# Kernel optimization log

Measured on AMD Instinct MI355X. Metric: run time of the kernel, lower is better.

The kernel has to match this reference:

```python
import jax, jax.numpy as jnp
import numpy as np


def _lstm(x, h0, c0, Wx, Wh, b):
    """Keras-order LSTM (gates i,f,c,o). x: [B,T,E] -> hidden seq [B,T,H]."""
    xw = jnp.einsum('bte,eg->btg', x, Wx) + b  # precompute input projections

    def step(carry, xw_t):
        h, c = carry
        z = xw_t + h @ Wh
        i, f, g, o = jnp.split(z, 4, axis=-1)
        c = jax.nn.sigmoid(f) * c + jax.nn.sigmoid(i) * jnp.tanh(g)
        h = jax.nn.sigmoid(o) * jnp.tanh(c)
        return (h, c), h

    _, hs = jax.lax.scan(step, (h0, c0), jnp.swapaxes(xw, 0, 1))
    return jnp.swapaxes(hs, 0, 1)


def setup_inputs() -> dict:
    key = jax.random.key(0)
    ks = jax.random.split(key, 16)
    V_IN = V_OUT = 32000
    E = 512      # embedding_dim
    H = 512      # encoder hidden_units per direction
    D = 2 * H    # decoder state width (matches BiLSTM output / attention dims)
    B, T_IN, T_OUT = 4, 128, 128
    s = 0.02

    def w(k, shape):
        return jax.random.normal(k, shape, jnp.float32) * s

    return {
        'input_seq': jax.random.randint(ks[0], (B, T_IN), 0, V_IN, jnp.int32),
        'output_seq': jax.random.randint(ks[1], (B, T_OUT), 0, V_OUT, jnp.int32),
        'enc_emb': w(ks[2], (V_IN, E)),
        'dec_emb': w(ks[3], (V_OUT, E)),
        'Wx_f': w(ks[4], (E, 4 * H)), 'Wh_f': w(ks[5], (H, 4 * H)), 'b_f': jnp.zeros((4 * H,), jnp.float32),
        'Wx_b': w(ks[6], (E, 4 * H)), 'Wh_b': w(ks[7], (H, 4 * H)), 'b_b': jnp.zeros((4 * H,), jnp.float32),
        'Wx_d': w(ks[8], (E, 4 * D)), 'Wh_d': w(ks[9], (D, 4 * D)), 'b_d': jnp.zeros((4 * D,), jnp.float32),
        'attn_scale': w(ks[10], (D,)),
        'Wo': w(ks[11], (D, V_OUT)), 'bo': jnp.zeros((V_OUT,), jnp.float32),
    }


def reference(input_seq, output_seq, enc_emb, dec_emb,
              Wx_f, Wh_f, b_f, Wx_b, Wh_b, b_b,
              Wx_d, Wh_d, b_d, attn_scale, Wo, bo):
    B = input_seq.shape[0]
    H = Wh_f.shape[0]
    D = 2 * H

    # --- encoder: BiLSTM, return_sequences=True ---
    enc_x = enc_emb[input_seq]                       # [B,Tin,E]
    z = jnp.zeros((B, H), jnp.float32)
    fwd = _lstm(enc_x, z, z, Wx_f, Wh_f, b_f)        # [B,Tin,H]
    bwd = _lstm(enc_x[:, ::-1], z, z, Wx_b, Wh_b, b_b)[:, ::-1]
    enc_out = jnp.concatenate([fwd, bwd], axis=-1)   # [B,Tin,2H]

    # --- decoder: LSTMCell-driven RNN, init state = last encoder output ---
    dec_x = dec_emb[output_seq]                      # [B,Tout,E]
    h0 = enc_out[:, -1, :]                           # [B,D]
    c0 = jnp.zeros((B, D), jnp.float32)
    dec_out = _lstm(dec_x, h0, c0, Wx_d, Wh_d, b_d)  # [B,Tout,D]

    # --- additive (Bahdanau) attention: query=dec_out, key=value=enc_out ---
    scores = jnp.einsum(
        'btsd,d->bts',
        jnp.tanh(dec_out[:, :, None, :] + enc_out[:, None, :, :]),
        attn_scale)                                  # [B,Tout,Tin]
    wts = jax.nn.softmax(scores, axis=-1)
    attn = jnp.einsum('bts,bsd->btd', wts, enc_out)  # [B,Tout,D]

    # --- output dense + softmax over vocab ---
    return jax.nn.softmax(attn @ Wo + bo, axis=-1)   # [B,Tout,V_out]
```

## Files before the change

kernel.cpp:

```cpp
#include <hip/hip_runtime.h>


typedef __attribute__((ext_vector_type(8))) short bf16x8;
typedef __attribute__((ext_vector_type(4))) float f32x4;

__device__ __forceinline__ short f2bf(float f) {
  unsigned u = __builtin_bit_cast(unsigned, f);
  u += 0x7fffu + ((u >> 16) & 1u);
  return (short)(u >> 16);
}
__device__ __forceinline__ float b2f(short s) {
  unsigned u = ((unsigned)(unsigned short)s) << 16;
  return __builtin_bit_cast(float, u);
}
__device__ __forceinline__ float sigf(float x) { return 1.f / (1.f + __expf(-x)); }
__device__ __forceinline__ float tanhf_fast(float x) {
  x = fminf(fmaxf(x, -15.f), 15.f);
  float e = __expf(2.f * x);
  return (e - 1.f) / (e + 1.f);
}

__device__ __forceinline__ unsigned ld_coh(const unsigned* p) {
  return __hip_atomic_load(p, __ATOMIC_RELAXED, __HIP_MEMORY_SCOPE_AGENT);
}
__device__ __forceinline__ void st_coh(unsigned* p, unsigned v) {
  __hip_atomic_store(p, v, __ATOMIC_RELAXED, __HIP_MEMORY_SCOPE_AGENT);
}

#define OFF_HBF   ((size_t)0)
#define OFF_HBB   (OFF_HBF + 2*2048*4)
#define OFF_HBD   (OFF_HBB + 2*2048*4)
#define OFF_ENCX  (OFF_HBD + 2*4096*4)
#define OFF_DECX  (OFF_ENCX + (size_t)64*512*8*2)
#define OFF_WXF   (OFF_DECX + (size_t)64*512*8*2)
#define OFF_WXB   (OFF_WXF + (size_t)512*2048*2)
#define OFF_WXD   (OFF_WXB + (size_t)512*2048*2)
#define OFF_WOS   (OFF_WXD + (size_t)512*4096*2)
#define OFF_XWF   (OFF_WOS + (size_t)1024*32000*2)
#define OFF_XWB   (OFF_XWF + (size_t)512*2048*4)
#define OFF_XWD   (OFF_XWB + (size_t)512*2048*4)
#define OFF_ENCO  (OFF_XWD + (size_t)512*4096*4)
#define OFF_ENCT  (OFF_ENCO + (size_t)4*128*1024*4)
#define OFF_DECO  (OFF_ENCT + (size_t)4*128*1024*4)
#define OFF_ATTN  (OFF_DECO + (size_t)4*128*1024*4)
#define OFF_LOG   (OFF_ATTN + (size_t)128*512*8*2)
#define WS_NEED   (OFF_LOG + (size_t)512*32000*2)

__device__ __forceinline__ void gather_body(const int* seq, const float* emb,
                                            short* dst, int bx, int by) {
  int m  = by * 64 + (threadIdx.x & 63);
  int e8 = bx * 4 + (threadIdx.x >> 6);
  int id = seq[m];
  const float* src = emb + (size_t)id * 512 + e8 * 8;
  bf16x8 v;
#pragma unroll
  for (int j = 0; j < 8; ++j) v[j] = f2bf(src[j]);
  *(bf16x8*)(dst + ((size_t)e8 * 512 + m) * 8) = v;
}

__device__ __forceinline__ void swz_body(const float* W, short* dst, int N,
                                         int k8, int n) {
  const float* src = W + (size_t)k8 * 8 * N + n;
  bf16x8 v;
#pragma unroll
  for (int j = 0; j < 8; ++j) v[j] = f2bf(src[(size_t)j * N]);
  *(bf16x8*)(dst + ((size_t)k8 * N + n) * 8) = v;
}

__device__ __forceinline__ void gemm_body(const short* __restrict__ A,
                                          const short* __restrict__ B,
                                          float* Cf, short* Cb,
                                          int M, int N, int K,
                                          int bx, int by, bool bf16out) {
  const int wv = threadIdx.x >> 6, lane = threadIdx.x & 63;
  const int q = lane >> 4, l15 = lane & 15;
  const int m0 = by * 128 + (wv >> 1) * 64;
  const int n0 = bx * 128 + (wv & 1) * 64;
  f32x4 acc[4][4];
#pragma unroll
  for (int i = 0; i < 4; ++i)
#pragma unroll
    for (int j = 0; j < 4; ++j) acc[i][j] = (f32x4){0.f, 0.f, 0.f, 0.f};
  const int KS = K >> 5;
  for (int ks = 0; ks < KS; ++ks) {
    const size_t k8 = (size_t)(ks * 4 + q);
    const short* Ap = A + (k8 * M + m0 + l15) * 8;
    const short* Bp = B + (k8 * N + n0 + l15) * 8;
    bf16x8 av[4], bv[4];
#pragma unroll
    for (int i = 0; i < 4; ++i) av[i] = *(const bf16x8*)(Ap + i * 128);
#pragma unroll
    for (int j = 0; j < 4; ++j) bv[j] = *(const bf16x8*)(Bp + j * 128);
#pragma unroll
    for (int i = 0; i < 4; ++i)
#pragma unroll
      for (int j = 0; j < 4; ++j)
        acc[i][j] = __builtin_amdgcn_mfma_f32_16x16x32_bf16(av[i], bv[j], acc[i][j], 0, 0, 0);
  }
#pragma unroll
  for (int i = 0; i < 4; ++i)
#pragma unroll
    for (int j = 0; j < 4; ++j)
#pragma unroll
      for (int r = 0; r < 4; ++r) {
        size_t idx = (size_t)(m0 + i * 16 + q * 4 + r) * N + (n0 + j * 16 + l15);
        if (bf16out) Cb[idx] = f2bf(acc[i][j][r]);
        else         Cf[idx] = acc[i][j][r];
      }
}

__global__ __launch_bounds__(256) void prep(
    const int* __restrict__ iseq, const int* __restrict__ oseq,
    const float* __restrict__ enc_emb, const float* __restrict__ dec_emb,
    const float* __restrict__ Wx_f, const float* __restrict__ Wx_b,
    const float* __restrict__ Wx_d,
    short* encx, short* decx, short* wxf_s, short* wxb_s, short* wxd_s) {
  int bid = blockIdx.x;
  if (bid < 128)        { gather_body(iseq, enc_emb, encx, bid & 15, bid >> 4); return; }
  if (bid < 256)        { int s = bid - 128;  gather_body(oseq, dec_emb, decx, s & 15, s >> 4); return; }
  if (bid < 768)        { int s = bid - 256;  swz_body(Wx_f, wxf_s, 2048, s >> 3, (s & 7) * 256 + threadIdx.x); return; }
  if (bid < 1280)       { int s = bid - 768;  swz_body(Wx_b, wxb_s, 2048, s >> 3, (s & 7) * 256 + threadIdx.x); return; }
  { int s = bid - 1280; swz_body(Wx_d, wxd_s, 4096, s >> 4, (s & 15) * 256 + threadIdx.x); }
}

__global__ __launch_bounds__(256) void xw_enc_gemm(
    const short* __restrict__ encx, const short* __restrict__ wxf_s,
    const short* __restrict__ wxb_s, float* xw_f, float* xw_b) {
  gemm_body(encx, blockIdx.z ? wxb_s : wxf_s, blockIdx.z ? xw_b : xw_f,
            nullptr, 512, 2048, 512, blockIdx.x, blockIdx.y, false);
}

__global__ __launch_bounds__(256, 1) void lstm_enc_fused(
    const float* __restrict__ Wh_f, const float* __restrict__ Wh_b,
    const float* __restrict__ xw_f, const float* __restrict__ xw_b,
    const float* __restrict__ b_f, const float* __restrict__ b_b,
    unsigned* hb_f, unsigned* hb_b, float* enc_out, float* encT,
    const short* __restrict__ decx, const short* __restrict__ wxd_s,
    float* xw_d, const float* __restrict__ Wo, short* wo_s) {
  const int bid = blockIdx.x;
  const int tid = threadIdx.x;
  if (bid >= 192) {
    int sb = bid - 192;
    int k8 = sb / 125, nb = sb - k8 * 125;
    swz_body(Wo, wo_s, 32000, k8, nb * 256 + tid);
    return;
  }
  if (bid >= 64) {
    int gb = bid - 64;
    gemm_body(decx, wxd_s, xw_d, nullptr, 512, 4096, 512, gb & 31, gb >> 5, false);
    return;
  }
  const int dir = bid >> 5;
  const int u0  = (bid & 31) * 16;
  const int w = tid >> 6, lane = tid & 63;
  const int q = lane >> 4, l15 = lane & 15;
  const float* Wh   = dir ? Wh_b : Wh_f;
  const float* xw   = dir ? xw_b : xw_f;
  const float* bias = dir ? b_b : b_f;
  unsigned* hb = dir ? hb_b : hb_f;

  __shared__ short hs[5][520];
  __shared__ float zb[4][4][16];
  __shared__ float cb[4][16];
  if (tid < 64) {
    cb[tid >> 4][tid & 15] = 0.f;
    st_coh(hb + (tid >> 4) * 512 + u0 + (tid & 15), 1u << 16);
  }
  for (int k = tid; k < 520; k += 256) hs[4][k] = 0;

  const int col = w * 512 + u0 + l15;
  const float bcol = bias[col];
  bf16x8 wfrag[16];
#pragma unroll
  for (int ks = 0; ks < 16; ++ks) {
    bf16x8 v;
#pragma unroll
    for (int jj = 0; jj < 8; ++jj) {
      int k = ks * 32 + q * 8 + jj;
      v[jj] = f2bf(Wh[(size_t)k * 2048 + col]);
    }
    wfrag[ks] = v;
  }
  const short* hp = hs[(l15 < 4) ? l15 : 4];
  float xwv[4];
  if (q == 0) {
    int tx0 = dir ? 127 : 0;
#pragma unroll
    for (int r = 0; r < 4; ++r) xwv[r] = xw[((size_t)(r * 128 + tx0)) * 2048 + col];
  }
  __syncthreads();

#pragma unroll 1
  for (int t = 0; t < 128; ++t) {
    const unsigned exp_ = (unsigned)(t + 1);
    const unsigned* src = hb + (t & 1) * 2048;
    unsigned v[8];
    bool ok;
    int guard = 0;
    do {
#pragma unroll
      for (int j = 0; j < 8; ++j) v[j] = ld_coh(src + j * 256 + tid);
      ok = true;
#pragma unroll
      for (int j = 0; j < 8; ++j) ok &= ((v[j] >> 16) == exp_);
      if (!ok) __builtin_amdgcn_s_sleep(1);
    } while (!ok && ++guard < (1 << 14));
#pragma unroll
    for (int j = 0; j < 8; ++j) {
      unsigned idx = j * 256 + tid;
      hs[idx >> 9][idx & 511] = (short)(v[j] & 0xffffu);
    }
    __syncthreads();

    f32x4 a0 = (f32x4){0.f, 0.f, 0.f, 0.f}, a1 = a0;
#pragma unroll
    for (int ks = 0; ks < 16; ks += 2) {
      bf16x8 f0 = *(const bf16x8*)(hp + ks * 32 + q * 8);
      bf16x8 f1 = *(const bf16x8*)(hp + (ks + 1) * 32 + q * 8);
      a0 = __builtin_amdgcn_mfma_f32_16x16x32_bf16(f0, wfrag[ks], a0, 0, 0, 0);
      a1 = __builtin_amdgcn_mfma_f32_16x16x32_bf16(f1, wfrag[ks + 1], a1, 0, 0, 0);
    }
    const int tx = dir ? (127 - t) : t;
    if (q == 0) {
#pragma unroll
      for (int r = 0; r < 4; ++r) zb[w][r][l15] = a0[r] + a1[r] + xwv[r] + bcol;
      if (t < 127) {
        int txn = dir ? (126 - t) : (t + 1);
#pragma unroll
        for (int r = 0; r < 4; ++r) xwv[r] = xw[((size_t)(r * 128 + txn)) * 2048 + col];
      }
    }
    __syncthreads();
    if (tid < 64) {
      int b = tid >> 4, u = tid & 15;
      float zi = zb[0][b][u], zf = zb[1][b][u], zg = zb[2][b][u], zo = zb[3][b][u];
      float c = sigf(zf) * cb[b][u] + sigf(zi) * tanhf_fast(zg);
      cb[b][u] = c;
      float h = sigf(zo) * tanhf_fast(c);
      if (t < 127)
        st_coh(hb + ((t + 1) & 1) * 2048 + b * 512 + u0 + u,
               ((unsigned)(t + 2) << 16) | (unsigned short)f2bf(h));
      int d = dir * 512 + u0 + u;
      enc_out[((size_t)(b * 128 + tx)) * 1024 + d] = h;
      encT[((size_t)(b * 1024 + d)) * 128 + tx] = h;
    }
  }
}

__global__ __launch_bounds__(256, 1) void lstm_dec(
    const float* __restrict__ Wh_d, const float* __restrict__ xw_d,
    const float* __restrict__ b_d, const float* __restrict__ enc_out,
    unsigned* hb, float* dec_out) {
  const int u0  = blockIdx.x * 16;
  const int tid = threadIdx.x;
  const int w = tid >> 6, lane = tid & 63;
  const int q = lane >> 4, l15 = lane & 15;

  __shared__ short hs[5][1032];
  __shared__ float zb[4][4][16];
  __shared__ float cb[4][16];
  if (tid < 64) {
    int b = tid >> 4, u = tid & 15;
    cb[b][u] = 0.f;
    float h0 = enc_out[((size_t)(b * 128 + 127)) * 1024 + u0 + u];
    st_coh(hb + b * 1024 + u0 + u, (1u << 16) | (unsigned short)f2bf(h0));
  }
  for (int k = tid; k < 1032; k += 256) hs[4][k] = 0;

  const int col = w * 1024 + u0 + l15;
  const float bcol = b_d[col];
  bf16x8 wfrag[32];
#pragma unroll
  for (int ks = 0; ks < 32; ++ks) {
    bf16x8 v;
#pragma unroll
    for (int jj = 0; jj < 8; ++jj) {
      int k = ks * 32 + q * 8 + jj;
      v[jj] = f2bf(Wh_d[(size_t)k * 4096 + col]);
    }
    wfrag[ks] = v;
  }
  const short* hp = hs[(l15 < 4) ? l15 : 4];
  float xwv[4];
  if (q == 0) {
#pragma unroll
    for (int r = 0; r < 4; ++r) xwv[r] = xw_d[((size_t)(r * 128)) * 4096 + col];
  }
  __syncthreads();

#pragma unroll 1
  for (int t = 0; t < 128; ++t) {
    const unsigned exp_ = (unsigned)(t + 1);
    const unsigned* src = hb + (t & 1) * 4096;
    unsigned v[16];
    bool ok;
    int guard = 0;
    do {
#pragma unroll
      for (int j = 0; j < 16; ++j) v[j] = ld_coh(src + j * 256 + tid);
      ok = true;
#pragma unroll
      for (int j = 0; j < 16; ++j) ok &= ((v[j] >> 16) == exp_);
      if (!ok) __builtin_amdgcn_s_sleep(1);
    } while (!ok && ++guard < (1 << 14));
#pragma unroll
    for (int j = 0; j < 16; ++j) {
      unsigned idx = j * 256 + tid;
      hs[idx >> 10][idx & 1023] = (short)(v[j] & 0xffffu);
    }
    __syncthreads();

    f32x4 a0 = (f32x4){0.f, 0.f, 0.f, 0.f}, a1 = a0;
#pragma unroll
    for (int ks = 0; ks < 32; ks += 2) {
      bf16x8 f0 = *(const bf16x8*)(hp + ks * 32 + q * 8);
      bf16x8 f1 = *(const bf16x8*)(hp + (ks + 1) * 32 + q * 8);
      a0 = __builtin_amdgcn_mfma_f32_16x16x32_bf16(f0, wfrag[ks], a0, 0, 0, 0);
      a1 = __builtin_amdgcn_mfma_f32_16x16x32_bf16(f1, wfrag[ks + 1], a1, 0, 0, 0);
    }
    if (q == 0) {
#pragma unroll
      for (int r = 0; r < 4; ++r) zb[w][r][l15] = a0[r] + a1[r] + xwv[r] + bcol;
      if (t < 127) {
#pragma unroll
        for (int r = 0; r < 4; ++r) xwv[r] = xw_d[((size_t)(r * 128 + t + 1)) * 4096 + col];
      }
    }
    __syncthreads();
    if (tid < 64) {
      int b = tid >> 4, u = tid & 15;
      float zi = zb[0][b][u], zf = zb[1][b][u], zg = zb[2][b][u], zo = zb[3][b][u];
      float c = sigf(zf) * cb[b][u] + sigf(zi) * tanhf_fast(zg);
      cb[b][u] = c;
      float h = sigf(zo) * tanhf_fast(c);
      if (t < 127)
        st_coh(hb + ((t + 1) & 1) * 4096 + b * 1024 + u0 + u,
               ((unsigned)(t + 2) << 16) | (unsigned short)f2bf(h));
      dec_out[((size_t)(b * 128 + t)) * 1024 + u0 + u] = h;
    }
  }
}

__global__ __launch_bounds__(256) void attention(
    const float* __restrict__ dec_out, const float* __restrict__ enc_out,
    const float* __restrict__ encT, const float* __restrict__ scale,
    short* __restrict__ attn_swz) {
  const int m = blockIdx.x, b = m >> 7, tid = threadIdx.x;
  __shared__ float dec_s[1024], scl_s[1024];
  __shared__ float red[256], wts[128], sred[2];
  for (int d = tid; d < 1024; d += 256) {
    dec_s[d] = dec_out[(size_t)m * 1024 + d];
    scl_s[d] = scale[d];
  }
  __syncthreads();
  const int s = tid & 127, half = tid >> 7;
  float sc = 0.f;
  const float* ep = encT + (size_t)b * 1024 * 128 + s;
  for (int d = half * 512; d < half * 512 + 512; ++d)
    sc += tanhf_fast(dec_s[d] + ep[(size_t)d * 128]) * scl_s[d];
  red[tid] = sc;
  __syncthreads();
  float v = 0.f;
  if (tid < 128) { v = red[tid] + red[tid + 128]; wts[tid] = v; }
  __syncthreads();
  if (tid < 64) {
    float mx = fmaxf(wts[tid], wts[tid + 64]);
    for (int off = 32; off; off >>= 1) mx = fmaxf(mx, __shfl_down(mx, off));
    if (tid == 0) sred[0] = mx;
  }
  __syncthreads();
  const float MX = sred[0];
  if (tid < 128) { v = __expf(v - MX); wts[tid] = v; }
  __syncthreads();
  if (tid < 64) {
    float sm = wts[tid] + wts[tid + 64];
    for (int off = 32; off; off >>= 1) sm += __shfl_down(sm, off);
    if (tid == 0) sred[1] = sm;
  }
  __syncthreads();
  const float inv = 1.f / sred[1];
  if (tid < 128) wts[tid] = v * inv;
  __syncthreads();
#pragma unroll
  for (int kk = 0; kk < 4; ++kk) {
    int d = tid + kk * 256;
    float a = 0.f;
    for (int ss = 0; ss < 128; ++ss)
      a += wts[ss] * enc_out[((size_t)(b * 128 + ss)) * 1024 + d];
    attn_swz[((size_t)(d >> 3) * 512 + m) * 8 + (d & 7)] = f2bf(a);
  }
}

__global__ __launch_bounds__(256) void gemm_wo(const short* __restrict__ attn_s,
                                               const short* __restrict__ wo_s,
                                               short* logits) {
  gemm_body(attn_s, wo_s, nullptr, logits, 512, 32000, 1024,
            blockIdx.x, blockIdx.y, true);
}

__global__ __launch_bounds__(256) void softmax_out(const short* __restrict__ logits,
                                                   const float* __restrict__ bo,
                                                   float* __restrict__ out) {
  const int m = blockIdx.x, tid = threadIdx.x;
  __shared__ float red[256];
  const short* lp = logits + (size_t)m * 32000;
  float mx = -1e30f;
  for (int n = tid; n < 32000; n += 256) mx = fmaxf(mx, b2f(lp[n]) + bo[n]);
  red[tid] = mx;
  __syncthreads();
  for (int s2 = 128; s2 > 0; s2 >>= 1) {
    if (tid < s2) red[tid] = fmaxf(red[tid], red[tid + s2]);
    __syncthreads();
  }
  const float M = red[0];
  __syncthreads();
  float sm = 0.f;
  for (int n = tid; n < 32000; n += 256) sm += __expf(b2f(lp[n]) + bo[n] - M);
  red[tid] = sm;
  __syncthreads();
  for (int s2 = 128; s2 > 0; s2 >>= 1) {
    if (tid < s2) red[tid] += red[tid + s2];
    __syncthreads();
  }
  const float inv = 1.f / red[0];
  for (int n = tid; n < 32000; n += 256)
    out[(size_t)m * 32000 + n] = __expf(b2f(lp[n]) + bo[n] - M) * inv;
}

extern "C" void kernel_launch(void* const* d_in, const int* in_sizes, int n_in,
                              void* d_out, int out_size, void* d_ws, size_t ws_size,
                              hipStream_t stream) {
  (void)in_sizes; (void)n_in; (void)out_size;
  if (ws_size < WS_NEED) return;

  const int*   input_seq  = (const int*)d_in[0];
  const int*   output_seq = (const int*)d_in[1];
  const float* enc_emb    = (const float*)d_in[2];
  const float* dec_emb    = (const float*)d_in[3];
  const float* Wx_f = (const float*)d_in[4];
  const float* Wh_f = (const float*)d_in[5];
  const float* b_f  = (const float*)d_in[6];
  const float* Wx_b = (const float*)d_in[7];
  const float* Wh_b = (const float*)d_in[8];
  const float* b_b  = (const float*)d_in[9];
  const float* Wx_d = (const float*)d_in[10];
  const float* Wh_d = (const float*)d_in[11];
  const float* b_d  = (const float*)d_in[12];
  const float* attn_scale = (const float*)d_in[13];
  const float* Wo   = (const float*)d_in[14];
  const float* bo   = (const float*)d_in[15];
  float* out = (float*)d_out;

  char* ws = (char*)d_ws;
  unsigned* hbf   = (unsigned*)(ws + OFF_HBF);
  unsigned* hbb   = (unsigned*)(ws + OFF_HBB);
  unsigned* hbd   = (unsigned*)(ws + OFF_HBD);
  short* encx     = (short*)(ws + OFF_ENCX);
  short* decx     = (short*)(ws + OFF_DECX);
  short* wxf_s    = (short*)(ws + OFF_WXF);
  short* wxb_s    = (short*)(ws + OFF_WXB);
  short* wxd_s    = (short*)(ws + OFF_WXD);
  short* wo_s     = (short*)(ws + OFF_WOS);
  float* xw_f     = (float*)(ws + OFF_XWF);
  float* xw_b     = (float*)(ws + OFF_XWB);
  float* xw_d     = (float*)(ws + OFF_XWD);
  float* enc_out  = (float*)(ws + OFF_ENCO);
  float* encT     = (float*)(ws + OFF_ENCT);
  float* dec_out  = (float*)(ws + OFF_DECO);
  short* attn_s   = (short*)(ws + OFF_ATTN);
  short* logits   = (short*)(ws + OFF_LOG);


  prep<<<2304, 256, 0, stream>>>(input_seq, output_seq, enc_emb, dec_emb,
                                 Wx_f, Wx_b, Wx_d, encx, decx, wxf_s, wxb_s, wxd_s);
  xw_enc_gemm<<<dim3(16, 4, 2), 256, 0, stream>>>(encx, wxf_s, wxb_s, xw_f, xw_b);
  lstm_enc_fused<<<64 + 128 + 16000, 256, 0, stream>>>(
      Wh_f, Wh_b, xw_f, xw_b, b_f, b_b, hbf, hbb, enc_out, encT,
      decx, wxd_s, xw_d, Wo, wo_s);
  lstm_dec<<<64, 256, 0, stream>>>(Wh_d, xw_d, b_d, enc_out, hbd, dec_out);
  attention<<<512, 256, 0, stream>>>(dec_out, enc_out, encT, attn_scale, attn_s);
  gemm_wo<<<dim3(250, 4), 256, 0, stream>>>(attn_s, wo_s, logits);
  softmax_out<<<512, 256, 0, stream>>>(logits, bo, out);
}
```

Measured before the change: 1.175 ms.

## Fuse input projections into LSTM kernels and overlap attention with decoder

Removes the separate input-projection GEMMs and weight swizzles. Each LSTM block now computes its own slice of x·Wx into shared memory before the recurrence. The gate column layout is remapped so each lane holds all four gates (i,f,g,o) for one unit and batch, which removes the zb shared-memory exchange and one __syncthreads per step. The poll loop is double-buffered, and the attention blocks run inside the decoder kernel, spinning on per-timestep published hidden states so attention overlaps the recurrence. The tradeoffs are a longer serial prologue per recurrent block, attention blocks spinning while they occupy CUs, and the risk of deadlock if they cannot all be co-resident with the 64 LSTM blocks.

```diff
diff --git a/kernel.cpp b/kernel.cpp
--- a/kernel.cpp
+++ b/kernel.cpp
@@ -19,7 +19,6 @@
   float e = __expf(2.f * x);
   return (e - 1.f) / (e + 1.f);
 }
-
 __device__ __forceinline__ unsigned ld_coh(const unsigned* p) {
   return __hip_atomic_load(p, __ATOMIC_RELAXED, __HIP_MEMORY_SCOPE_AGENT);
 }
@@ -28,21 +27,15 @@
 }
 
 #define OFF_HBF   ((size_t)0)
-#define OFF_HBB   (OFF_HBF + 2*2048*4)
-#define OFF_HBD   (OFF_HBB + 2*2048*4)
-#define OFF_ENCX  (OFF_HBD + 2*4096*4)
+#define OFF_HBB   (OFF_HBF + (size_t)2*2048*4)
+#define OFF_HBD   (OFF_HBB + (size_t)2*2048*4)
+#define OFF_HBH   (OFF_HBD + (size_t)2*4096*4)
+#define OFF_ENCX  (OFF_HBH + (size_t)128*4*1024*4)
 #define OFF_DECX  (OFF_ENCX + (size_t)64*512*8*2)
-#define OFF_WXF   (OFF_DECX + (size_t)64*512*8*2)
-#define OFF_WXB   (OFF_WXF + (size_t)512*2048*2)
-#define OFF_WXD   (OFF_WXB + (size_t)512*2048*2)
-#define OFF_WOS   (OFF_WXD + (size_t)512*4096*2)
-#define OFF_XWF   (OFF_WOS + (size_t)1024*32000*2)
-#define OFF_XWB   (OFF_XWF + (size_t)512*2048*4)
-#define OFF_XWD   (OFF_XWB + (size_t)512*2048*4)
-#define OFF_ENCO  (OFF_XWD + (size_t)512*4096*4)
+#define OFF_WOS   (OFF_DECX + (size_t)64*512*8*2)
+#define OFF_ENCO  (OFF_WOS + (size_t)1024*32000*2)
 #define OFF_ENCT  (OFF_ENCO + (size_t)4*128*1024*4)
-#define OFF_DECO  (OFF_ENCT + (size_t)4*128*1024*4)
-#define OFF_ATTN  (OFF_DECO + (size_t)4*128*1024*4)
+#define OFF_ATTN  (OFF_ENCT + (size_t)4*128*1024*4)
 #define OFF_LOG   (OFF_ATTN + (size_t)128*512*8*2)
 #define WS_NEED   (OFF_LOG + (size_t)512*32000*2)
 
@@ -67,22 +60,333 @@
   *(bf16x8*)(dst + ((size_t)k8 * N + n) * 8) = v;
 }
 
-__device__ __forceinline__ void gemm_body(const short* __restrict__ A,
-                                          const short* __restrict__ B,
-                                          float* Cf, short* Cb,
-                                          int M, int N, int K,
-                                          int bx, int by, bool bf16out) {
+__global__ __launch_bounds__(256) void prep(const int* __restrict__ iseq,
+                                            const int* __restrict__ oseq,
+                                            const float* __restrict__ enc_emb,
+                                            const float* __restrict__ dec_emb,
+                                            short* encx, short* decx) {
+  int bid = blockIdx.x;
+  if (bid < 128) gather_body(iseq, enc_emb, encx, bid & 15, bid >> 4);
+  else { int s = bid - 128; gather_body(oseq, dec_emb, decx, s & 15, s >> 4); }
+}
+
+__global__ __launch_bounds__(256, 1) void lstm_enc_fused(
+    const float* __restrict__ Wh_f, const float* __restrict__ Wh_b,
+    const float* __restrict__ Wx_f, const float* __restrict__ Wx_b,
+    const float* __restrict__ b_f, const float* __restrict__ b_b,
+    const short* __restrict__ encx,
+    unsigned* hb_f, unsigned* hb_b, float* enc_out, float* encT,
+    const float* __restrict__ Wo, short* wo_s) {
+  const int bid = blockIdx.x, tid = threadIdx.x;
+  if (bid >= 64) {
+    int sb = bid - 64;
+    int k8 = sb / 125, nb = sb - k8 * 125;
+    swz_body(Wo, wo_s, 32000, k8, nb * 256 + tid);
+    return;
+  }
+  __shared__ float xws[512][16];
+  __shared__ short hs[4][528];
+  const int dir = bid >> 5, u0 = (bid & 31) * 16;
+  const int w = tid >> 6, lane = tid & 63, q = lane >> 4, l15 = lane & 15;
+  const int bq = l15 & 3;
+  const int unit = u0 + w * 4 + q;
+  unsigned* hb = dir ? hb_b : hb_f;
+
+  if (l15 < 4) st_coh(hb + l15 * 512 + unit, 1u << 16);
+
+  const int colA = (l15 & 3) * 512 + u0 + w * 4 + (l15 >> 2);
+  const float* Wx   = dir ? Wx_b : Wx_f;
+  const float* bias = dir ? b_b : b_f;
+  const float bcol = bias[colA];
+
+  {
+    bf16x8 bfr[16];
+#pragma unroll
+    for (int ks = 0; ks < 16; ++ks) {
+      bf16x8 v;
+#pragma unroll
+      for (int jj = 0; jj < 8; ++jj)
+        v[jj] = f2bf(Wx[(size_t)(ks * 32 + q * 8 + jj) * 2048 + colA]);
+      bfr[ks] = v;
+    }
+    for (int mt = 0; mt < 32; ++mt) {
+      f32x4 a0 = {0.f,0.f,0.f,0.f}, a1 = a0;
+#pragma unroll
+      for (int ks = 0; ks < 16; ks += 2) {
+        bf16x8 f0 = *(const bf16x8*)(encx + ((size_t)(ks*4 + q) * 512 + mt*16 + l15) * 8);
+        bf16x8 f1 = *(const bf16x8*)(encx + ((size_t)((ks+1)*4 + q) * 512 + mt*16 + l15) * 8);
+        a0 = __builtin_amdgcn_mfma_f32_16x16x32_bf16(f0, bfr[ks], a0, 0, 0, 0);
+        a1 = __builtin_amdgcn_mfma_f32_16x16x32_bf16(f1, bfr[ks+1], a1, 0, 0, 0);
+      }
+#pragma unroll
+      for (int r = 0; r < 4; ++r) xws[mt*16 + q*4 + r][l15] = a0[r] + a1[r] + bcol;
+    }
+  }
+  const float* Wh = dir ? Wh_b : Wh_f;
+  bf16x8 wfrag[16];
+#pragma unroll
+  for (int ks = 0; ks < 16; ++ks) {
+    bf16x8 v;
+#pragma unroll
+    for (int jj = 0; jj < 8; ++jj)
+      v[jj] = f2bf(Wh[(size_t)(ks * 32 + q * 8 + jj) * 2048 + colA]);
+    wfrag[ks] = v;
+  }
+  __syncthreads();
+  float creg = 0.f;
+  f32x4 xwv = *(const f32x4*)&xws[bq * 128 + (dir ? 127 : 0)][q * 4];
+
+#pragma unroll 1
+  for (int t = 0; t < 128; ++t) {
+    const unsigned exp_ = (unsigned)(t + 1);
+    const unsigned* src = hb + (t & 1) * 2048;
+    unsigned pa[8], pb[8];
+#pragma unroll
+    for (int j = 0; j < 8; ++j) pa[j] = ld_coh(src + j * 256 + tid);
+#pragma unroll
+    for (int j = 0; j < 8; ++j) pb[j] = ld_coh(src + j * 256 + tid);
+    int guard = 0;
+    for (;;) {
+      bool ok = true;
+#pragma unroll
+      for (int j = 0; j < 8; ++j) ok &= (pa[j] >> 16) == exp_;
+      if (ok || ++guard > (1 << 16)) break;
+#pragma unroll
+      for (int j = 0; j < 8; ++j) pa[j] = pb[j];
+#pragma unroll
+      for (int j = 0; j < 8; ++j) pb[j] = ld_coh(src + j * 256 + tid);
+    }
+#pragma unroll
+    for (int j = 0; j < 8; ++j) {
+      int idx = j * 256 + tid;
+      hs[idx >> 9][idx & 511] = (short)(pa[j] & 0xffffu);
+    }
+    __syncthreads();
+
+    f32x4 a0 = {0.f,0.f,0.f,0.f}, a1 = a0, a2 = a0, a3 = a0;
+    const short* hrow = hs[bq];
+#pragma unroll
+    for (int ks = 0; ks < 16; ks += 4) {
+      bf16x8 h0 = *(const bf16x8*)(hrow + ks * 32 + q * 8);
+      bf16x8 h1 = *(const bf16x8*)(hrow + (ks+1) * 32 + q * 8);
+      bf16x8 h2 = *(const bf16x8*)(hrow + (ks+2) * 32 + q * 8);
+      bf16x8 h3 = *(const bf16x8*)(hrow + (ks+3) * 32 + q * 8);
+      a0 = __builtin_amdgcn_mfma_f32_16x16x32_bf16(wfrag[ks],   h0, a0, 0, 0, 0);
+      a1 = __builtin_amdgcn_mfma_f32_16x16x32_bf16(wfrag[ks+1], h1, a1, 0, 0, 0);
+      a2 = __builtin_amdgcn_mfma_f32_16x16x32_bf16(wfrag[ks+2], h2, a2, 0, 0, 0);
+      a3 = __builtin_amdgcn_mfma_f32_16x16x32_bf16(wfrag[ks+3], h3, a3, 0, 0, 0);
+    }
+    const int tx = dir ? (127 - t) : t;
+    if (l15 < 4) {
+      const int b = l15;
+      float zi = a0[0] + a1[0] + a2[0] + a3[0] + xwv[0];
+      float zf = a0[1] + a1[1] + a2[1] + a3[1] + xwv[1];
+      float zg = a0[2] + a1[2] + a2[2] + a3[2] + xwv[2];
+      float zo = a0[3] + a1[3] + a2[3] + a3[3] + xwv[3];
+      float cst = sigf(zf) * creg + sigf(zi) * tanhf_fast(zg);
+      creg = cst;
+      float h = sigf(zo) * tanhf_fast(cst);
+      if (t < 127)
+        st_coh(hb + ((t + 1) & 1) * 2048 + b * 512 + unit,
+               ((unsigned)(t + 2) << 16) | (unsigned short)f2bf(h));
+      const int d = dir * 512 + unit;
+      enc_out[((size_t)(b * 128 + tx)) * 1024 + d] = h;
+      encT[((size_t)(b * 1024 + d)) * 128 + tx] = h;
+    }
+    if (t < 127)
+      xwv = *(const f32x4*)&xws[bq * 128 + (dir ? 126 - t : t + 1)][q * 4];
+  }
+}
+
+struct DecL { float xws[512][16]; short hs[4][1056]; };
+struct DecA { float dec_s[1024]; float scl[1024]; float red[256]; float wts[128]; float sred[2]; };
+
+__global__ __launch_bounds__(256, 1) void lstm_dec_fused(
+    const float* __restrict__ Wh_d, const float* __restrict__ Wx_d,
+    const float* __restrict__ b_d, const short* __restrict__ decx,
+    const float* __restrict__ enc_out, const float* __restrict__ encT,
+    const float* __restrict__ scale,
+    unsigned* hb, unsigned* hbh, short* attn_swz) {
+  const int bid = blockIdx.x, tid = threadIdx.x;
+  __shared__ union { DecL l; DecA a; } sh;
+
+  if (bid >= 64) {
+    const int m = bid - 64, b = m >> 7, t = m & 127;
+    const unsigned exp_ = (unsigned)(t + 2);
+    const unsigned* src = hbh + ((size_t)t * 4 + b) * 1024;
+    float* dec_s = sh.a.dec_s; float* scl_s = sh.a.scl;
+    float* red = sh.a.red; float* wts = sh.a.wts; float* sred = sh.a.sred;
+#pragma unroll
+    for (int kk = 0; kk < 4; ++kk) {
+      int d = tid + kk * 256;
+      unsigned v = ld_coh(src + d);
+      int g = 0;
+      while ((v >> 16) != exp_) {
+        __builtin_amdgcn_s_sleep(64);
+        v = ld_coh(src + d);
+        if (++g > (1 << 13)) break;
+      }
+      dec_s[d] = b2f((short)(v & 0xffffu));
+      scl_s[d] = scale[d];
+    }
+    __syncthreads();
+    const int s = tid & 127, half = tid >> 7;
+    float sc = 0.f;
+    const float* ep = encT + (size_t)b * 1024 * 128 + s;
+    for (int d = half * 512; d < half * 512 + 512; ++d)
+      sc += tanhf_fast(dec_s[d] + ep[(size_t)d * 128]) * scl_s[d];
+    red[tid] = sc;
+    __syncthreads();
+    float v = 0.f;
+    if (tid < 128) { v = red[tid] + red[tid + 128]; wts[tid] = v; }
+    __syncthreads();
+    if (tid < 64) {
+      float mx = fmaxf(wts[tid], wts[tid + 64]);
+      for (int off = 32; off; off >>= 1) mx = fmaxf(mx, __shfl_down(mx, off));
+      if (tid == 0) sred[0] = mx;
+    }
+    __syncthreads();
+    const float MX = sred[0];
+    if (tid < 128) { v = __expf(v - MX); wts[tid] = v; }
+    __syncthreads();
+    if (tid < 64) {
+      float sm = wts[tid] + wts[tid + 64];
+      for (int off = 32; off; off >>= 1) sm += __shfl_down(sm, off);
+      if (tid == 0) sred[1] = sm;
+    }
+    __syncthreads();
+    const float inv = 1.f / sred[1];
+    if (tid < 128) wts[tid] = v * inv;
+    __syncthreads();
+#pragma unroll
+    for (int kk = 0; kk < 4; ++kk) {
+      int d = tid + kk * 256;
+      float a = 0.f;
+      for (int ss = 0; ss < 128; ++ss)
+        a += wts[ss] * enc_out[((size_t)(b * 128 + ss)) * 1024 + d];
+      attn_swz[((size_t)(d >> 3) * 512 + m) * 8 + (d & 7)] = f2bf(a);
+    }
+    return;
+  }
+  const int u0 = bid * 16;
+  const int w = tid >> 6, lane = tid & 63, q = lane >> 4, l15 = lane & 15;
+  const int bq = l15 & 3;
+  const int unit = u0 + w * 4 + q;
+
+  if (l15 < 4)
+    st_coh(hb + l15 * 1024 + unit,
+           (1u << 16) |
+           (unsigned short)f2bf(enc_out[((size_t)(l15 * 128 + 127)) * 1024 + unit]));
+
+  const int colA = (l15 & 3) * 1024 + u0 + w * 4 + (l15 >> 2);
+  const float bcol = b_d[colA];
+  {
+    bf16x8 bfr[16];
+#pragma unroll
+    for (int ks = 0; ks < 16; ++ks) {
+      bf16x8 v;
+#pragma unroll
+      for (int jj = 0; jj < 8; ++jj)
+        v[jj] = f2bf(Wx_d[(size_t)(ks * 32 + q * 8 + jj) * 4096 + colA]);
+      bfr[ks] = v;
+    }
+    for (int mt = 0; mt < 32; ++mt) {
+      f32x4 a0 = {0.f,0.f,0.f,0.f}, a1 = a0;
+#pragma unroll
+      for (int ks = 0; ks < 16; ks += 2) {
+        bf16x8 f0 = *(const bf16x8*)(decx + ((size_t)(ks*4 + q) * 512 + mt*16 + l15) * 8);
+        bf16x8 f1 = *(const bf16x8*)(decx + ((size_t)((ks+1)*4 + q) * 512 + mt*16 + l15) * 8);
+        a0 = __builtin_amdgcn_mfma_f32_16x16x32_bf16(f0, bfr[ks], a0, 0, 0, 0);
+        a1 = __builtin_amdgcn_mfma_f32_16x16x32_bf16(f1, bfr[ks+1], a1, 0, 0, 0);
+      }
+#pragma unroll
+      for (int r = 0; r < 4; ++r) sh.l.xws[mt*16 + q*4 + r][l15] = a0[r] + a1[r] + bcol;
+    }
+  }
+  bf16x8 wfrag[32];
+#pragma unroll
+  for (int ks = 0; ks < 32; ++ks) {
+    bf16x8 v;
+#pragma unroll
+    for (int jj = 0; jj < 8; ++jj)
+      v[jj] = f2bf(Wh_d[(size_t)(ks * 32 + q * 8 + jj) * 4096 + colA]);
+    wfrag[ks] = v;
+  }
+  __syncthreads();
+  float creg = 0.f;
+  f32x4 xwv = *(const f32x4*)&sh.l.xws[bq * 128][q * 4];
+
+#pragma unroll 1
+  for (int t = 0; t < 128; ++t) {
+    const unsigned exp_ = (unsigned)(t + 1);
+    const unsigned* src = hb + (t & 1) * 4096;
+    unsigned pa[16], pb[16];
+#pragma unroll
+    for (int j = 0; j < 16; ++j) pa[j] = ld_coh(src + j * 256 + tid);
+#pragma unroll
+    for (int j = 0; j < 16; ++j) pb[j] = ld_coh(src + j * 256 + tid);
+    int guard = 0;
+    for (;;) {
+      bool ok = true;
+#pragma unroll
+      for (int j = 0; j < 16; ++j) ok &= (pa[j] >> 16) == exp_;
+      if (ok || ++guard > (1 << 16)) break;
+#pragma unroll
+      for (int j = 0; j < 16; ++j) pa[j] = pb[j];
+#pragma unroll
+      for (int j = 0; j < 16; ++j) pb[j] = ld_coh(src + j * 256 + tid);
+    }
+#pragma unroll
+    for (int j = 0; j < 16; ++j) {
+      int idx = j * 256 + tid;
+      sh.l.hs[idx >> 10][idx & 1023] = (short)(pa[j] & 0xffffu);
+    }
+    __syncthreads();
+
+    f32x4 a0 = {0.f,0.f,0.f,0.f}, a1 = a0, a2 = a0, a3 = a0;
+    const short* hrow = sh.l.hs[bq];
+#pragma unroll
+    for (int ks = 0; ks < 32; ks += 4) {
+      bf16x8 h0 = *(const bf16x8*)(hrow + ks * 32 + q * 8);
+      bf16x8 h1 = *(const bf16x8*)(hrow + (ks+1) * 32 + q * 8);
+      bf16x8 h2 = *(const bf16x8*)(hrow + (ks+2) * 32 + q * 8);
+      bf16x8 h3 = *(const bf16x8*)(hrow + (ks+3) * 32 + q * 8);
+      a0 = __builtin_amdgcn_mfma_f32_16x16x32_bf16(wfrag[ks],   h0, a0, 0, 0, 0);
+      a1 = __builtin_amdgcn_mfma_f32_16x16x32_bf16(wfrag[ks+1], h1, a1, 0, 0, 0);
+      a2 = __builtin_amdgcn_mfma_f32_16x16x32_bf16(wfrag[ks+2], h2, a2, 0, 0, 0);
+      a3 = __builtin_amdgcn_mfma_f32_16x16x32_bf16(wfrag[ks+3], h3, a3, 0, 0, 0);
+    }
+    if (l15 < 4) {
+      const int b = l15;
+      float zi = a0[0] + a1[0] + a2[0] + a3[0] + xwv[0];
+      float zf = a0[1] + a1[1] + a2[1] + a3[1] + xwv[1];
+      float zg = a0[2] + a1[2] + a2[2] + a3[2] + xwv[2];
+      float zo = a0[3] + a1[3] + a2[3] + a3[3] + xwv[3];
+      float cst = sigf(zf) * creg + sigf(zi) * tanhf_fast(zg);
+      creg = cst;
+      float h = sigf(zo) * tanhf_fast(cst);
+      unsigned word = ((unsigned)(t + 2) << 16) | (unsigned short)f2bf(h);
+      if (t < 127) st_coh(hb + ((t + 1) & 1) * 4096 + b * 1024 + unit, word);
+      st_coh(hbh + ((size_t)t * 4 + b) * 1024 + unit, word);
+    }
+    if (t < 127) xwv = *(const f32x4*)&sh.l.xws[bq * 128 + t + 1][q * 4];
+  }
+}
+
+__global__ __launch_bounds__(256) void gemm_wo(const short* __restrict__ A,
+                                               const short* __restrict__ B,
+                                               short* __restrict__ Cb) {
   const int wv = threadIdx.x >> 6, lane = threadIdx.x & 63;
   const int q = lane >> 4, l15 = lane & 15;
-  const int m0 = by * 128 + (wv >> 1) * 64;
-  const int n0 = bx * 128 + (wv & 1) * 64;
+  const int m0 = blockIdx.y * 128 + (wv >> 1) * 64;
+  const int n0 = blockIdx.x * 128 + (wv & 1) * 64;
+  const int M = 512, N = 32000;
   f32x4 acc[4][4];
 #pragma unroll
   for (int i = 0; i < 4; ++i)
 #pragma unroll
     for (int j = 0; j < 4; ++j) acc[i][j] = (f32x4){0.f, 0.f, 0.f, 0.f};
-  const int KS = K >> 5;
-  for (int ks = 0; ks < KS; ++ks) {
+  for (int ks = 0; ks < 32; ++ks) {
     const size_t k8 = (size_t)(ks * 4 + q);
     const short* Ap = A + (k8 * M + m0 + l15) * 8;
     const short* Bp = B + (k8 * N + n0 + l15) * 8;
@@ -102,300 +406,8 @@
 #pragma unroll
     for (int j = 0; j < 4; ++j)
 #pragma unroll
-      for (int r = 0; r < 4; ++r) {
-        size_t idx = (size_t)(m0 + i * 16 + q * 4 + r) * N + (n0 + j * 16 + l15);
-        if (bf16out) Cb[idx] = f2bf(acc[i][j][r]);
-        else         Cf[idx] = acc[i][j][r];
-      }
-}
-
-__global__ __launch_bounds__(256) void prep(
-    const int* __restrict__ iseq, const int* __restrict__ oseq,
-    const float* __restrict__ enc_emb, const float* __restrict__ dec_emb,
-    const float* __restrict__ Wx_f, const float* __restrict__ Wx_b,
-    const float* __restrict__ Wx_d,
-    short* encx, short* decx, short* wxf_s, short* wxb_s, short* wxd_s) {
-  int bid = blockIdx.x;
-  if (bid < 128)        { gather_body(iseq, enc_emb, encx, bid & 15, bid >> 4); return; }
-  if (bid < 256)        { int s = bid - 128;  gather_body(oseq, dec_emb, decx, s & 15, s >> 4); return; }
-  if (bid < 768)        { int s = bid - 256;  swz_body(Wx_f, wxf_s, 2048, s >> 3, (s & 7) * 256 + threadIdx.x); return; }
-  if (bid < 1280)       { int s = bid - 768;  swz_body(Wx_b, wxb_s, 2048, s >> 3, (s & 7) * 256 + threadIdx.x); return; }
-  { int s = bid - 1280; swz_body(Wx_d, wxd_s, 4096, s >> 4, (s & 15) * 256 + threadIdx.x); }
-}
-
-__global__ __launch_bounds__(256) void xw_enc_gemm(
-    const short* __restrict__ encx, const short* __restrict__ wxf_s,
-    const short* __restrict__ wxb_s, float* xw_f, float* xw_b) {
-  gemm_body(encx, blockIdx.z ? wxb_s : wxf_s, blockIdx.z ? xw_b : xw_f,
-            nullptr, 512, 2048, 512, blockIdx.x, blockIdx.y, false);
-}
-
-__global__ __launch_bounds__(256, 1) void lstm_enc_fused(
-    const float* __restrict__ Wh_f, const float* __restrict__ Wh_b,
-    const float* __restrict__ xw_f, const float* __restrict__ xw_b,
-    const float* __restrict__ b_f, const float* __restrict__ b_b,
-    unsigned* hb_f, unsigned* hb_b, float* enc_out, float* encT,
-    const short* __restrict__ decx, const short* __restrict__ wxd_s,
-    float* xw_d, const float* __restrict__ Wo, short* wo_s) {
-  const int bid = blockIdx.x;
-  const int tid = threadIdx.x;
-  if (bid >= 192) {
-    int sb = bid - 192;
-    int k8 = sb / 125, nb = sb - k8 * 125;
-    swz_body(Wo, wo_s, 32000, k8, nb * 256 + tid);
-    return;
-  }
-  if (bid >= 64) {
-    int gb = bid - 64;
-    gemm_body(decx, wxd_s, xw_d, nullptr, 512, 4096, 512, gb & 31, gb >> 5, false);
-    return;
-  }
-  const int dir = bid >> 5;
-  const int u0  = (bid & 31) * 16;
-  const int w = tid >> 6, lane = tid & 63;
-  const int q = lane >> 4, l15 = lane & 15;
-  const float* Wh   = dir ? Wh_b : Wh_f;
-  const float* xw   = dir ? xw_b : xw_f;
-  const float* bias = dir ? b_b : b_f;
-  unsigned* hb = dir ? hb_b : hb_f;
-
-  __shared__ short hs[5][520];
-  __shared__ float zb[4][4][16];
-  __shared__ float cb[4][16];
-  if (tid < 64) {
-    cb[tid >> 4][tid & 15] = 0.f;
-    st_coh(hb + (tid >> 4) * 512 + u0 + (tid & 15), 1u << 16);
-  }
-  for (int k = tid; k < 520; k += 256) hs[4][k] = 0;
-
-  const int col = w * 512 + u0 + l15;
-  const float bcol = bias[col];
-  bf16x8 wfrag[16];
-#pragma unroll
-  for (int ks = 0; ks < 16; ++ks) {
-    bf16x8 v;
-#pragma unroll
-    for (int jj = 0; jj < 8; ++jj) {
-      int k = ks * 32 + q * 8 + jj;
-      v[jj] = f2bf(Wh[(size_t)k * 2048 + col]);
-    }
-    wfrag[ks] = v;
-  }
-  const short* hp = hs[(l15 < 4) ? l15 : 4];
-  float xwv[4];
-  if (q == 0) {
-    int tx0 = dir ? 127 : 0;
-#pragma unroll
-    for (int r = 0; r < 4; ++r) xwv[r] = xw[((size_t)(r * 128 + tx0)) * 2048 + col];
-  }
-  __syncthreads();
-
-#pragma unroll 1
-  for (int t = 0; t < 128; ++t) {
-    const unsigned exp_ = (unsigned)(t + 1);
-    const unsigned* src = hb + (t & 1) * 2048;
-    unsigned v[8];
-    bool ok;
-    int guard = 0;
-    do {
-#pragma unroll
-      for (int j = 0; j < 8; ++j) v[j] = ld_coh(src + j * 256 + tid);
-      ok = true;
-#pragma unroll
-      for (int j = 0; j < 8; ++j) ok &= ((v[j] >> 16) == exp_);
-      if (!ok) __builtin_amdgcn_s_sleep(1);
-    } while (!ok && ++guard < (1 << 14));
-#pragma unroll
-    for (int j = 0; j < 8; ++j) {
-      unsigned idx = j * 256 + tid;
-      hs[idx >> 9][idx & 511] = (short)(v[j] & 0xffffu);
-    }
-    __syncthreads();
-
-    f32x4 a0 = (f32x4){0.f, 0.f, 0.f, 0.f}, a1 = a0;
-#pragma unroll
-    for (int ks = 0; ks < 16; ks += 2) {
-      bf16x8 f0 = *(const bf16x8*)(hp + ks * 32 + q * 8);
-      bf16x8 f1 = *(const bf16x8*)(hp + (ks + 1) * 32 + q * 8);
-      a0 = __builtin_amdgcn_mfma_f32_16x16x32_bf16(f0, wfrag[ks], a0, 0, 0, 0);
-      a1 = __builtin_amdgcn_mfma_f32_16x16x32_bf16(f1, wfrag[ks + 1], a1, 0, 0, 0);
-    }
-    const int tx = dir ? (127 - t) : t;
-    if (q == 0) {
-#pragma unroll
-      for (int r = 0; r < 4; ++r) zb[w][r][l15] = a0[r] + a1[r] + xwv[r] + bcol;
-      if (t < 127) {
-        int txn = dir ? (126 - t) : (t + 1);
-#pragma unroll
-        for (int r = 0; r < 4; ++r) xwv[r] = xw[((size_t)(r * 128 + txn)) * 2048 + col];
-      }
-    }
-    __syncthreads();
-    if (tid < 64) {
-      int b = tid >> 4, u = tid & 15;
-      float zi = zb[0][b][u], zf = zb[1][b][u], zg = zb[2][b][u], zo = zb[3][b][u];
-      float c = sigf(zf) * cb[b][u] + sigf(zi) * tanhf_fast(zg);
-      cb[b][u] = c;
-      float h = sigf(zo) * tanhf_fast(c);
-      if (t < 127)
-        st_coh(hb + ((t + 1) & 1) * 2048 + b * 512 + u0 + u,
-               ((unsigned)(t + 2) << 16) | (unsigned short)f2bf(h));
-      int d = dir * 512 + u0 + u;
-      enc_out[((size_t)(b * 128 + tx)) * 1024 + d] = h;
-      encT[((size_t)(b * 1024 + d)) * 128 + tx] = h;
-    }
-  }
-}
-
-__global__ __launch_bounds__(256, 1) void lstm_dec(
-    const float* __restrict__ Wh_d, const float* __restrict__ xw_d,
-    const float* __restrict__ b_d, const float* __restrict__ enc_out,
-    unsigned* hb, float* dec_out) {
-  const int u0  = blockIdx.x * 16;
-  const int tid = threadIdx.x;
-  const int w = tid >> 6, lane = tid & 63;
-  const int q = lane >> 4, l15 = lane & 15;
-
-  __shared__ short hs[5][1032];
-  __shared__ float zb[4][4][16];
-  __shared__ float cb[4][16];
-  if (tid < 64) {
-    int b = tid >> 4, u = tid & 15;
-    cb[b][u] = 0.f;
-    float h0 = enc_out[((size_t)(b * 128 + 127)) * 1024 + u0 + u];
-    st_coh(hb + b * 1024 + u0 + u, (1u << 16) | (unsigned short)f2bf(h0));
-  }
-  for (int k = tid; k < 1032; k += 256) hs[4][k] = 0;
-
-  const int col = w * 1024 + u0 + l15;
-  const float bcol = b_d[col];
-  bf16x8 wfrag[32];
-#pragma unroll
-  for (int ks = 0; ks < 32; ++ks) {
-    bf16x8 v;
-#pragma unroll
-    for (int jj = 0; jj < 8; ++jj) {
-      int k = ks * 32 + q * 8 + jj;
-      v[jj] = f2bf(Wh_d[(size_t)k * 4096 + col]);
-    }
-    wfrag[ks] = v;
-  }
-  const short* hp = hs[(l15 < 4) ? l15 : 4];
-  float xwv[4];
-  if (q == 0) {
-#pragma unroll
-    for (int r = 0; r < 4; ++r) xwv[r] = xw_d[((size_t)(r * 128)) * 4096 + col];
-  }
-  __syncthreads();
-
-#pragma unroll 1
-  for (int t = 0; t < 128; ++t) {
-    const unsigned exp_ = (unsigned)(t + 1);
-    const unsigned* src = hb + (t & 1) * 4096;
-    unsigned v[16];
-    bool ok;
-    int guard = 0;
-    do {
-#pragma unroll
-      for (int j = 0; j < 16; ++j) v[j] = ld_coh(src + j * 256 + tid);
-      ok = true;
-#pragma unroll
-      for (int j = 0; j < 16; ++j) ok &= ((v[j] >> 16) == exp_);
-      if (!ok) __builtin_amdgcn_s_sleep(1);
-    } while (!ok && ++guard < (1 << 14));
-#pragma unroll
-    for (int j = 0; j < 16; ++j) {
-      unsigned idx = j * 256 + tid;
-      hs[idx >> 10][idx & 1023] = (short)(v[j] & 0xffffu);
-    }
-    __syncthreads();
-
-    f32x4 a0 = (f32x4){0.f, 0.f, 0.f, 0.f}, a1 = a0;
-#pragma unroll
-    for (int ks = 0; ks < 32; ks += 2) {
-      bf16x8 f0 = *(const bf16x8*)(hp + ks * 32 + q * 8);
-      bf16x8 f1 = *(const bf16x8*)(hp + (ks + 1) * 32 + q * 8);
-      a0 = __builtin_amdgcn_mfma_f32_16x16x32_bf16(f0, wfrag[ks], a0, 0, 0, 0);
-      a1 = __builtin_amdgcn_mfma_f32_16x16x32_bf16(f1, wfrag[ks + 1], a1, 0, 0, 0);
-    }
-    if (q == 0) {
-#pragma unroll
-      for (int r = 0; r < 4; ++r) zb[w][r][l15] = a0[r] + a1[r] + xwv[r] + bcol;
-      if (t < 127) {
-#pragma unroll
-        for (int r = 0; r < 4; ++r) xwv[r] = xw_d[((size_t)(r * 128 + t + 1)) * 4096 + col];
-      }
-    }
-    __syncthreads();
-    if (tid < 64) {
-      int b = tid >> 4, u = tid & 15;
-      float zi = zb[0][b][u], zf = zb[1][b][u], zg = zb[2][b][u], zo = zb[3][b][u];
-      float c = sigf(zf) * cb[b][u] + sigf(zi) * tanhf_fast(zg);
-      cb[b][u] = c;
-      float h = sigf(zo) * tanhf_fast(c);
-      if (t < 127)
-        st_coh(hb + ((t + 1) & 1) * 4096 + b * 1024 + u0 + u,
-               ((unsigned)(t + 2) << 16) | (unsigned short)f2bf(h));
-      dec_out[((size_t)(b * 128 + t)) * 1024 + u0 + u] = h;
-    }
-  }
-}
-
-__global__ __launch_bounds__(256) void attention(
-    const float* __restrict__ dec_out, const float* __restrict__ enc_out,
-    const float* __restrict__ encT, const float* __restrict__ scale,
-    short* __restrict__ attn_swz) {
-  const int m = blockIdx.x, b = m >> 7, tid = threadIdx.x;
-  __shared__ float dec_s[1024], scl_s[1024];
-  __shared__ float red[256], wts[128], sred[2];
-  for (int d = tid; d < 1024; d += 256) {
-    dec_s[d] = dec_out[(size_t)m * 1024 + d];
-    scl_s[d] = scale[d];
-  }
-  __syncthreads();
-  const int s = tid & 127, half = tid >> 7;
-  float sc = 0.f;
-  const float* ep = encT + (size_t)b * 1024 * 128 + s;
-  for (int d = half * 512; d < half * 512 + 512; ++d)
-    sc += tanhf_fast(dec_s[d] + ep[(size_t)d * 128]) * scl_s[d];
-  red[tid] = sc;
-  __syncthreads();
-  float v = 0.f;
-  if (tid < 128) { v = red[tid] + red[tid + 128]; wts[tid] = v; }
-  __syncthreads();
-  if (tid < 64) {
-    float mx = fmaxf(wts[tid], wts[tid + 64]);
-    for (int off = 32; off; off >>= 1) mx = fmaxf(mx, __shfl_down(mx, off));
-    if (tid == 0) sred[0] = mx;
-  }
-  __syncthreads();
-  const float MX = sred[0];
-  if (tid < 128) { v = __expf(v - MX); wts[tid] = v; }
-  __syncthreads();
-  if (tid < 64) {
-    float sm = wts[tid] + wts[tid + 64];
-    for (int off = 32; off; off >>= 1) sm += __shfl_down(sm, off);
-    if (tid == 0) sred[1] = sm;
-  }
-  __syncthreads();
-  const float inv = 1.f / sred[1];
-  if (tid < 128) wts[tid] = v * inv;
-  __syncthreads();
-#pragma unroll
-  for (int kk = 0; kk < 4; ++kk) {
-    int d = tid + kk * 256;
-    float a = 0.f;
-    for (int ss = 0; ss < 128; ++ss)
-      a += wts[ss] * enc_out[((size_t)(b * 128 + ss)) * 1024 + d];
-    attn_swz[((size_t)(d >> 3) * 512 + m) * 8 + (d & 7)] = f2bf(a);
-  }
-}
-
-__global__ __launch_bounds__(256) void gemm_wo(const short* __restrict__ attn_s,
-                                               const short* __restrict__ wo_s,
-                                               short* logits) {
-  gemm_body(attn_s, wo_s, nullptr, logits, 512, 32000, 1024,
-            blockIdx.x, blockIdx.y, true);
+      for (int r = 0; r < 4; ++r)
+        Cb[(size_t)(m0 + i * 16 + q * 4 + r) * N + (n0 + j * 16 + l15)] = f2bf(acc[i][j][r]);
 }
 
 __global__ __launch_bounds__(256) void softmax_out(const short* __restrict__ logits,
@@ -455,30 +467,21 @@
   unsigned* hbf   = (unsigned*)(ws + OFF_HBF);
   unsigned* hbb   = (unsigned*)(ws + OFF_HBB);
   unsigned* hbd   = (unsigned*)(ws + OFF_HBD);
+  unsigned* hbh   = (unsigned*)(ws + OFF_HBH);
   short* encx     = (short*)(ws + OFF_ENCX);
   short* decx     = (short*)(ws + OFF_DECX);
-  short* wxf_s    = (short*)(ws + OFF_WXF);
-  short* wxb_s    = (short*)(ws + OFF_WXB);
-  short* wxd_s    = (short*)(ws + OFF_WXD);
   short* wo_s     = (short*)(ws + OFF_WOS);
-  float* xw_f     = (float*)(ws + OFF_XWF);
-  float* xw_b     = (float*)(ws + OFF_XWB);
-  float* xw_d     = (float*)(ws + OFF_XWD);
   float* enc_out  = (float*)(ws + OFF_ENCO);
   float* encT     = (float*)(ws + OFF_ENCT);
-  float* dec_out  = (float*)(ws + OFF_DECO);
   short* attn_s   = (short*)(ws + OFF_ATTN);
   short* logits   = (short*)(ws + OFF_LOG);
 
 
-  prep<<<2304, 256, 0, stream>>>(input_seq, output_seq, enc_emb, dec_emb,
-                                 Wx_f, Wx_b, Wx_d, encx, decx, wxf_s, wxb_s, wxd_s);
-  xw_enc_gemm<<<dim3(16, 4, 2), 256, 0, stream>>>(encx, wxf_s, wxb_s, xw_f, xw_b);
-  lstm_enc_fused<<<64 + 128 + 16000, 256, 0, stream>>>(
-      Wh_f, Wh_b, xw_f, xw_b, b_f, b_b, hbf, hbb, enc_out, encT,
-      decx, wxd_s, xw_d, Wo, wo_s);
-  lstm_dec<<<64, 256, 0, stream>>>(Wh_d, xw_d, b_d, enc_out, hbd, dec_out);
-  attention<<<512, 256, 0, stream>>>(dec_out, enc_out, encT, attn_scale, attn_s);
+  prep<<<256, 256, 0, stream>>>(input_seq, output_seq, enc_emb, dec_emb, encx, decx);
+  lstm_enc_fused<<<64 + 16000, 256, 0, stream>>>(
+      Wh_f, Wh_b, Wx_f, Wx_b, b_f, b_b, encx, hbf, hbb, enc_out, encT, Wo, wo_s);
+  lstm_dec_fused<<<64 + 512, 256, 0, stream>>>(
+      Wh_d, Wx_d, b_d, decx, enc_out, encT, attn_scale, hbd, hbh, attn_s);
   gemm_wo<<<dim3(250, 4), 256, 0, stream>>>(attn_s, wo_s, logits);
   softmax_out<<<512, 256, 0, stream>>>(logits, bo, out);
 }
```

After: 1.554 ms. +32.3%, slower.
